# Optimization experiments

Hardware: AMD Instinct MI355X
Metric: run time of the kernel (lower is better)

The kernel has to match this reference:

```python
import jax, jax.numpy as jnp
import numpy as np


def setup_inputs() -> dict:
    key = jax.random.key(0)
    k1, k2 = jax.random.split(key)
    B, C, H, W = 16, 128, 32, 32   # C == embedding_dim
    K = 2048                        # codebook size (num_embeddings)
    x = jax.random.normal(k1, (B, C, H, W), dtype=jnp.float32)
    codebook = jax.random.normal(k2, (K, C), dtype=jnp.float32)
    return {"x": x, "codebook": codebook}


def reference(x, codebook):
    # x: [B, C, H, W] -> NHWC -> flatten to [N, C]
    B, C, H, W = x.shape
    x_nhwc = jnp.transpose(x, (0, 2, 3, 1))
    x_flat = x_nhwc.reshape(-1, C)                      # [N, C]
    # Squared L2 distances via expansion (argmin-equivalent to torch.norm
    # of the broadcast difference, without the [N, K, C] intermediate):
    x_sq = jnp.sum(x_flat * x_flat, axis=1, keepdims=True)   # [N, 1]
    w_sq = jnp.sum(codebook * codebook, axis=1)              # [K]
    d2 = x_sq - 2.0 * (x_flat @ codebook.T) + w_sq           # [N, K]
    encoding_indices = jnp.argmin(d2, axis=1)                # [N]
    encodings = jax.nn.one_hot(encoding_indices, codebook.shape[0],
                               dtype=x_flat.dtype)           # [N, K]
    quantized = encodings @ codebook                         # [N, C]
    quantized = jnp.transpose(quantized.reshape(B, H, W, C), (0, 3, 1, 2))
    return encodings, quantized
```

## Files before the change

### kernel.cpp

```cpp
#include <hip/hip_runtime.h>
#include <hip/hip_bf16.h>

#define N_TOK  16384
#define KCODES 2048
#define CDIM   128
#define BM     64
#define TPB    512
#define NCW    4
#define CPW    (KCODES / NCW)
#define TPW    (CPW / 16)
#define CAP    40
#define DELTA  5.0f
#define ASTR   68

typedef __attribute__((ext_vector_type(8))) short bhalf8;
typedef __attribute__((ext_vector_type(4))) float facc4;

__global__ __launch_bounds__(256) void prep_kernel(const float* __restrict__ cb,
                                                   bhalf8* __restrict__ cbt,
                                                   float* __restrict__ wsq) {
    const int T   = blockIdx.x;
    const int tid = threadIdx.x;
    const int r   = tid >> 4;
    const int g   = tid & 15;
    const float4* src = (const float4*)(cb + ((size_t)(T * 16 + r)) * CDIM + g * 8);
    float4 a0 = src[0], a1 = src[1];

    float s = a0.x*a0.x + a0.y*a0.y + a0.z*a0.z + a0.w*a0.w
            + a1.x*a1.x + a1.y*a1.y + a1.z*a1.z + a1.w*a1.w;
    s += __shfl_xor(s, 1, 64);
    s += __shfl_xor(s, 2, 64);
    s += __shfl_xor(s, 4, 64);
    s += __shfl_xor(s, 8, 64);
    if (g == 0) wsq[T * 16 + r] = s;

    union { unsigned u[4]; bhalf8 v; } fu;
    __hip_bfloat162 h0 = __float22bfloat162_rn(make_float2(a0.x, a0.y));
    __hip_bfloat162 h1 = __float22bfloat162_rn(make_float2(a0.z, a0.w));
    __hip_bfloat162 h2 = __float22bfloat162_rn(make_float2(a1.x, a1.y));
    __hip_bfloat162 h3 = __float22bfloat162_rn(make_float2(a1.z, a1.w));
    fu.u[0] = *(unsigned*)&h0; fu.u[1] = *(unsigned*)&h1;
    fu.u[2] = *(unsigned*)&h2; fu.u[3] = *(unsigned*)&h3;
    const int kf = g >> 2, q = g & 3;
    cbt[(size_t)T * 256 + kf * 64 + q * 16 + r] = fu.v;
}

__global__ __launch_bounds__(TPB, 1) void argmin_kernel(const float* __restrict__ x,
                                                        const float* __restrict__ cb,
                                                        const bhalf8* __restrict__ cbt,
                                                        const float* __restrict__ wsqg,
                                                        float* __restrict__ enc,
                                                        float* __restrict__ quant) {
    __shared__ float As[CDIM][ASTR];
    __shared__ float wsqs[KCODES];
    __shared__ float redvw[NCW][BM];
    __shared__ float rowthr[BM];
    __shared__ int   cnt[BM];
    __shared__ int   candk[BM][CAP];
    __shared__ int   rowidx[BM];

    const int tid  = threadIdx.x;
    const int lane = tid & 63;
    const int w    = tid >> 6;
    const int q    = lane >> 4;
    const int r    = lane & 15;
    const int n0   = blockIdx.x * BM;
    const int b    = n0 >> 10;
    const int hw0  = n0 & 1023;
    const float4 z4 = {0.f, 0.f, 0.f, 0.f};

    {
        int m4 = (tid & 15) << 2;
        int c0 = tid >> 4;
        #pragma unroll
        for (int i = 0; i < 4; i++) {
            int c = c0 + 32 * i;
            float4 v = *(const float4*)(x + (((size_t)(b * CDIM + c)) << 10) + hw0 + m4);
            *(float4*)(&As[c][m4]) = v;
        }
    }
    #pragma unroll
    for (int i = 0; i < KCODES / TPB; i++) wsqs[i * TPB + tid] = wsqg[i * TPB + tid];
    if (tid < BM) cnt[tid] = 0;
    __syncthreads();

    bhalf8 af[4][4];
    if (w < NCW) {
        #pragma unroll
        for (int rt = 0; rt < 4; rt++) {
            int m = rt * 16 + r;
            #pragma unroll
            for (int kf = 0; kf < 4; kf++) {
                union { unsigned u[4]; bhalf8 v; } fu;
                #pragma unroll
                for (int p = 0; p < 4; p++) {
                    int k = kf * 32 + q * 8 + 2 * p;
                    __hip_bfloat162 h = __float22bfloat162_rn(make_float2(As[k][m], As[k + 1][m]));
                    fu.u[p] = *(unsigned*)&h;
                }
                af[rt][kf] = fu.v;
            }
        }
    }

    const int    cw  = w * CPW;
    const size_t tb0 = (size_t)(cw >> 4) * 256;

    if (w < NCW) {
        float rmin[16];
        #pragma unroll
        for (int t = 0; t < 16; t++) rmin[t] = 3.0e38f;

        bhalf8 bcur[4], bnxt[4];
        #pragma unroll
        for (int kf = 0; kf < 4; kf++) bcur[kf] = cbt[tb0 + kf * 64 + lane];
        #pragma unroll
        for (int kf = 0; kf < 4; kf++) bnxt[kf] = cbt[tb0 + 256 + kf * 64 + lane];

        for (int t = 0; t < TPW; t++) {
            bhalf8 bn2[4];
            if (t + 2 < TPW) {
                size_t tb = tb0 + (size_t)(t + 2) * 256;
                #pragma unroll
                for (int kf = 0; kf < 4; kf++) bn2[kf] = cbt[tb + kf * 64 + lane];
            }
            facc4 acc[4];
            #pragma unroll
            for (int rt = 0; rt < 4; rt++) acc[rt] = (facc4){0.f, 0.f, 0.f, 0.f};
            #pragma unroll
            for (int kf = 0; kf < 4; kf++)
                #pragma unroll
                for (int rt = 0; rt < 4; rt++)
                    acc[rt] = __builtin_amdgcn_mfma_f32_16x16x32_bf16(af[rt][kf], bcur[kf], acc[rt], 0, 0, 0);
            float wv = wsqs[cw + t * 16 + r];
            #pragma unroll
            for (int rt = 0; rt < 4; rt++)
                #pragma unroll
                for (int i = 0; i < 4; i++)
                    rmin[rt * 4 + i] = fminf(rmin[rt * 4 + i], fmaf(-2.f, acc[rt][i], wv));
            #pragma unroll
            for (int kf = 0; kf < 4; kf++) { bcur[kf] = bnxt[kf]; bnxt[kf] = bn2[kf]; }
        }
        #pragma unroll
        for (int t = 0; t < 16; t++) {
            float v = rmin[t];
            v = fminf(v, __shfl_xor(v, 1, 64));
            v = fminf(v, __shfl_xor(v, 2, 64));
            v = fminf(v, __shfl_xor(v, 4, 64));
            v = fminf(v, __shfl_xor(v, 8, 64));
            if (r == 0) redvw[w][(t >> 2) * 16 + q * 4 + (t & 3)] = v;
        }
    } else {
        const int f = w - NCW;
        float4* dst = (float4*)(enc + (size_t)(n0 + f * 16) * KCODES);
        #pragma unroll 8
        for (int i = 0; i < 64; i++) dst[(size_t)i * 64 + lane] = z4;
    }
    __syncthreads();
    if (tid < BM) {
        float mv = fminf(fminf(redvw[0][tid], redvw[1][tid]),
                         fminf(redvw[2][tid], redvw[3][tid]));
        rowthr[tid] = mv + DELTA;
    }
    __syncthreads();

    if (w < NCW) {
        float thr[16];
        #pragma unroll
        for (int t = 0; t < 16; t++) thr[t] = rowthr[(t >> 2) * 16 + q * 4 + (t & 3)];

        bhalf8 bcur[4], bnxt[4];
        #pragma unroll
        for (int kf = 0; kf < 4; kf++) bcur[kf] = cbt[tb0 + kf * 64 + lane];
        #pragma unroll
        for (int kf = 0; kf < 4; kf++) bnxt[kf] = cbt[tb0 + 256 + kf * 64 + lane];

        for (int t = 0; t < TPW; t++) {
            bhalf8 bn2[4];
            if (t + 2 < TPW) {
                size_t tb = tb0 + (size_t)(t + 2) * 256;
                #pragma unroll
                for (int kf = 0; kf < 4; kf++) bn2[kf] = cbt[tb + kf * 64 + lane];
            }
            facc4 acc[4];
            #pragma unroll
            for (int rt = 0; rt < 4; rt++) acc[rt] = (facc4){0.f, 0.f, 0.f, 0.f};
            #pragma unroll
            for (int kf = 0; kf < 4; kf++)
                #pragma unroll
                for (int rt = 0; rt < 4; rt++)
                    acc[rt] = __builtin_amdgcn_mfma_f32_16x16x32_bf16(af[rt][kf], bcur[kf], acc[rt], 0, 0, 0);
            float wv = wsqs[cw + t * 16 + r];
            #pragma unroll
            for (int rt = 0; rt < 4; rt++)
                #pragma unroll
                for (int i = 0; i < 4; i++) {
                    float d = fmaf(-2.f, acc[rt][i], wv);
                    if (d <= thr[rt * 4 + i]) {
                        int row = rt * 16 + q * 4 + i;
                        int p = atomicAdd(&cnt[row], 1);
                        if (p < CAP) candk[row][p] = cw + t * 16 + r;
                    }
                }
            #pragma unroll
            for (int kf = 0; kf < 4; kf++) { bcur[kf] = bnxt[kf]; bnxt[kf] = bn2[kf]; }
        }
    } else {
        const int f = w - NCW;
        float4* dst = (float4*)(enc + (size_t)(n0 + f * 16) * KCODES);
        #pragma unroll 8
        for (int i = 64; i < 128; i++) dst[(size_t)i * 64 + lane] = z4;
    }
    __syncthreads();

    for (int m = 8 * w; m < 8 * w + 8; m++) {
        int c = min(cnt[m], CAP);
        float bv = 3.0e38f; int bk = 0x7fffffff;
        for (int t = 0; t < c; t++) {
            int k = candk[m][t];
            float x0 = As[lane][m], x1 = As[lane + 64][m];
            float c0 = cb[(size_t)k * CDIM + lane];
            float c1 = cb[(size_t)k * CDIM + 64 + lane];
            float s = x0 * c0 + x1 * c1;
            #pragma unroll
            for (int off = 1; off <= 32; off <<= 1) s += __shfl_xor(s, off, 64);
            float d = fmaf(-2.f, s, wsqs[k]);
            if (d < bv || (d == bv && k < bk)) { bv = d; bk = k; }
        }
        if (lane == 0) rowidx[m] = bk;
    }
    __syncthreads();

    if (tid < BM) enc[(size_t)(n0 + tid) * KCODES + rowidx[tid]] = 1.0f;

    #pragma unroll
    for (int i = tid; i < BM * CDIM / 4; i += TPB) {
        int c  = i >> 4;
        int hq = (i & 15) << 2;
        float4 v;
        v.x = cb[(size_t)rowidx[hq + 0] * CDIM + c];
        v.y = cb[(size_t)rowidx[hq + 1] * CDIM + c];
        v.z = cb[(size_t)rowidx[hq + 2] * CDIM + c];
        v.w = cb[(size_t)rowidx[hq + 3] * CDIM + c];
        *(float4*)(quant + (((size_t)(b * CDIM + c)) << 10) + hw0 + hq) = v;
    }
}

extern "C" void kernel_launch(void* const* d_in, const int* in_sizes, int n_in,
                              void* d_out, int out_size, void* d_ws, size_t ws_size,
                              hipStream_t stream) {
    const float* x  = (const float*)d_in[0];
    const float* cb = (const float*)d_in[1];
    float* out = (float*)d_out;

    bhalf8* cbt  = (bhalf8*)d_ws;
    float*  wsqp = (float*)((char*)d_ws + 512 * 1024);

    prep_kernel<<<KCODES / 16, 256, 0, stream>>>(cb, cbt, wsqp);
    argmin_kernel<<<N_TOK / BM, TPB, 0, stream>>>(x, cb, cbt, wsqp,
                                                  out, out + (size_t)N_TOK * KCODES);
}
```

Baseline: 191.3 us.

## Decouple zero-fill waves from compute waves with shared-memory flags instead of block barriers

The four zero-fill waves now write the whole one-hot matrix with nontemporal stores, then spin on a shared flag and write the ones themselves. The compute waves sync only among themselves through atomic counters, so the fill no longer stalls them at block barriers. The change also deepens codebook prefetch to four tiles with a fully unrolled loop and computes fp32 refinement distances one candidate per lane rather than with shuffle reductions. In exchange it relies on spin-waits in shared memory, raises register pressure, and lifts the candidate cap with more shared memory.

```diff
diff --git a/kernel.cpp b/kernel.cpp
--- a/kernel.cpp
+++ b/kernel.cpp
@@ -9,12 +9,13 @@
 #define NCW    4
 #define CPW    (KCODES / NCW)
 #define TPW    (CPW / 16)
-#define CAP    40
+#define CAP    48
 #define DELTA  5.0f
 #define ASTR   68
 
 typedef __attribute__((ext_vector_type(8))) short bhalf8;
 typedef __attribute__((ext_vector_type(4))) float facc4;
+typedef __attribute__((ext_vector_type(4))) float nf4;
 
 __global__ __launch_bounds__(256) void prep_kernel(const float* __restrict__ cb,
                                                    bhalf8* __restrict__ cbt,
@@ -54,10 +55,11 @@
     __shared__ float As[CDIM][ASTR];
     __shared__ float wsqs[KCODES];
     __shared__ float redvw[NCW][BM];
-    __shared__ float rowthr[BM];
     __shared__ int   cnt[BM];
     __shared__ int   candk[BM][CAP];
+    __shared__ float candd[BM][CAP];
     __shared__ int   rowidx[BM];
+    __shared__ int   cflag0, cflag1, cflag2, rflag;
 
     const int tid  = threadIdx.x;
     const int lane = tid & 63;
@@ -67,63 +69,77 @@
     const int n0   = blockIdx.x * BM;
     const int b    = n0 >> 10;
     const int hw0  = n0 & 1023;
-    const float4 z4 = {0.f, 0.f, 0.f, 0.f};
+
+    if (tid < BM) cnt[tid] = 0;
+    if (tid == 0) { cflag0 = 0; cflag1 = 0; cflag2 = 0; rflag = 0; }
+    __syncthreads();
+
+    if (w >= NCW) {
+        const int f = w - NCW;
+        nf4* dst = (nf4*)(enc + (size_t)(n0 + f * 16) * KCODES);
+        const nf4 z4 = {0.f, 0.f, 0.f, 0.f};
+        #pragma unroll 8
+        for (int i = 0; i < 128; i++)
+            __builtin_nontemporal_store(z4, dst + (size_t)i * 64 + lane);
+        __threadfence();
+        while (*(volatile int*)&rflag < NCW) __builtin_amdgcn_s_sleep(2);
+        __threadfence_block();
+        if (lane < 16) {
+            int m = f * 16 + lane;
+            enc[(size_t)(n0 + m) * KCODES + rowidx[m]] = 1.0f;
+        }
+        return;
+    }
 
     {
         int m4 = (tid & 15) << 2;
         int c0 = tid >> 4;
         #pragma unroll
-        for (int i = 0; i < 4; i++) {
-            int c = c0 + 32 * i;
+        for (int i = 0; i < 8; i++) {
+            int c = c0 + 16 * i;
             float4 v = *(const float4*)(x + (((size_t)(b * CDIM + c)) << 10) + hw0 + m4);
             *(float4*)(&As[c][m4]) = v;
         }
-    }
-    #pragma unroll
-    for (int i = 0; i < KCODES / TPB; i++) wsqs[i * TPB + tid] = wsqg[i * TPB + tid];
-    if (tid < BM) cnt[tid] = 0;
-    __syncthreads();
+        #pragma unroll
+        for (int i = 0; i < 8; i++) wsqs[i * 256 + tid] = wsqg[i * 256 + tid];
+    }
+    __threadfence_block();
+    if (lane == 0) atomicAdd(&cflag0, 1);
+    while (*(volatile int*)&cflag0 < NCW) __builtin_amdgcn_s_sleep(1);
+    __threadfence_block();
 
     bhalf8 af[4][4];
-    if (w < NCW) {
-        #pragma unroll
-        for (int rt = 0; rt < 4; rt++) {
-            int m = rt * 16 + r;
-            #pragma unroll
-            for (int kf = 0; kf < 4; kf++) {
-                union { unsigned u[4]; bhalf8 v; } fu;
-                #pragma unroll
-                for (int p = 0; p < 4; p++) {
-                    int k = kf * 32 + q * 8 + 2 * p;
-                    __hip_bfloat162 h = __float22bfloat162_rn(make_float2(As[k][m], As[k + 1][m]));
-                    fu.u[p] = *(unsigned*)&h;
-                }
-                af[rt][kf] = fu.v;
-            }
+    #pragma unroll
+    for (int rt = 0; rt < 4; rt++) {
+        int m = rt * 16 + r;
+        #pragma unroll
+        for (int kf = 0; kf < 4; kf++) {
+            union { unsigned u[4]; bhalf8 v; } fu;
+            #pragma unroll
+            for (int p = 0; p < 4; p++) {
+                int k = kf * 32 + q * 8 + 2 * p;
+                __hip_bfloat162 h = __float22bfloat162_rn(make_float2(As[k][m], As[k + 1][m]));
+                fu.u[p] = *(unsigned*)&h;
+            }
+            af[rt][kf] = fu.v;
         }
     }
 
     const int    cw  = w * CPW;
     const size_t tb0 = (size_t)(cw >> 4) * 256;
 
-    if (w < NCW) {
-        float rmin[16];
-        #pragma unroll
-        for (int t = 0; t < 16; t++) rmin[t] = 3.0e38f;
-
-        bhalf8 bcur[4], bnxt[4];
-        #pragma unroll
-        for (int kf = 0; kf < 4; kf++) bcur[kf] = cbt[tb0 + kf * 64 + lane];
-        #pragma unroll
-        for (int kf = 0; kf < 4; kf++) bnxt[kf] = cbt[tb0 + 256 + kf * 64 + lane];
-
+    float rmin[16];
+    #pragma unroll
+    for (int t = 0; t < 16; t++) rmin[t] = 3.0e38f;
+    {
+        bhalf8 bb[4][4];
+        #pragma unroll
+        for (int d = 0; d < 4; d++)
+            #pragma unroll
+            for (int kf = 0; kf < 4; kf++)
+                bb[d][kf] = cbt[tb0 + (size_t)d * 256 + kf * 64 + lane];
+        #pragma unroll
         for (int t = 0; t < TPW; t++) {
-            bhalf8 bn2[4];
-            if (t + 2 < TPW) {
-                size_t tb = tb0 + (size_t)(t + 2) * 256;
-                #pragma unroll
-                for (int kf = 0; kf < 4; kf++) bn2[kf] = cbt[tb + kf * 64 + lane];
-            }
             facc4 acc[4];
             #pragma unroll
             for (int rt = 0; rt < 4; rt++) acc[rt] = (facc4){0.f, 0.f, 0.f, 0.f};
@@ -131,57 +147,51 @@
             for (int kf = 0; kf < 4; kf++)
                 #pragma unroll
                 for (int rt = 0; rt < 4; rt++)
-                    acc[rt] = __builtin_amdgcn_mfma_f32_16x16x32_bf16(af[rt][kf], bcur[kf], acc[rt], 0, 0, 0);
+                    acc[rt] = __builtin_amdgcn_mfma_f32_16x16x32_bf16(af[rt][kf], bb[t & 3][kf], acc[rt], 0, 0, 0);
             float wv = wsqs[cw + t * 16 + r];
             #pragma unroll
             for (int rt = 0; rt < 4; rt++)
                 #pragma unroll
                 for (int i = 0; i < 4; i++)
                     rmin[rt * 4 + i] = fminf(rmin[rt * 4 + i], fmaf(-2.f, acc[rt][i], wv));
-            #pragma unroll
-            for (int kf = 0; kf < 4; kf++) { bcur[kf] = bnxt[kf]; bnxt[kf] = bn2[kf]; }
-        }
-        #pragma unroll
-        for (int t = 0; t < 16; t++) {
-            float v = rmin[t];
-            v = fminf(v, __shfl_xor(v, 1, 64));
-            v = fminf(v, __shfl_xor(v, 2, 64));
-            v = fminf(v, __shfl_xor(v, 4, 64));
-            v = fminf(v, __shfl_xor(v, 8, 64));
-            if (r == 0) redvw[w][(t >> 2) * 16 + q * 4 + (t & 3)] = v;
-        }
-    } else {
-        const int f = w - NCW;
-        float4* dst = (float4*)(enc + (size_t)(n0 + f * 16) * KCODES);
-        #pragma unroll 8
-        for (int i = 0; i < 64; i++) dst[(size_t)i * 64 + lane] = z4;
-    }
-    __syncthreads();
-    if (tid < BM) {
-        float mv = fminf(fminf(redvw[0][tid], redvw[1][tid]),
-                         fminf(redvw[2][tid], redvw[3][tid]));
-        rowthr[tid] = mv + DELTA;
-    }
-    __syncthreads();
-
-    if (w < NCW) {
-        float thr[16];
-        #pragma unroll
-        for (int t = 0; t < 16; t++) thr[t] = rowthr[(t >> 2) * 16 + q * 4 + (t & 3)];
-
-        bhalf8 bcur[4], bnxt[4];
-        #pragma unroll
-        for (int kf = 0; kf < 4; kf++) bcur[kf] = cbt[tb0 + kf * 64 + lane];
-        #pragma unroll
-        for (int kf = 0; kf < 4; kf++) bnxt[kf] = cbt[tb0 + 256 + kf * 64 + lane];
-
+            if (t + 4 < TPW) {
+                #pragma unroll
+                for (int kf = 0; kf < 4; kf++)
+                    bb[t & 3][kf] = cbt[tb0 + (size_t)(t + 4) * 256 + kf * 64 + lane];
+            }
+        }
+    }
+    #pragma unroll
+    for (int t = 0; t < 16; t++) {
+        float v = rmin[t];
+        v = fminf(v, __shfl_xor(v, 1, 64));
+        v = fminf(v, __shfl_xor(v, 2, 64));
+        v = fminf(v, __shfl_xor(v, 4, 64));
+        v = fminf(v, __shfl_xor(v, 8, 64));
+        if (r == 0) redvw[w][(t >> 2) * 16 + q * 4 + (t & 3)] = v;
+    }
+    __threadfence_block();
+    if (lane == 0) atomicAdd(&cflag1, 1);
+    while (*(volatile int*)&cflag1 < NCW) __builtin_amdgcn_s_sleep(1);
+    __threadfence_block();
+
+    float thr[16];
+    #pragma unroll
+    for (int t = 0; t < 16; t++) {
+        int rm = (t >> 2) * 16 + q * 4 + (t & 3);
+        thr[t] = fminf(fminf(redvw[0][rm], redvw[1][rm]),
+                       fminf(redvw[2][rm], redvw[3][rm])) + DELTA;
+    }
+
+    {
+        bhalf8 bb[4][4];
+        #pragma unroll
+        for (int d = 0; d < 4; d++)
+            #pragma unroll
+            for (int kf = 0; kf < 4; kf++)
+                bb[d][kf] = cbt[tb0 + (size_t)d * 256 + kf * 64 + lane];
+        #pragma unroll
         for (int t = 0; t < TPW; t++) {
-            bhalf8 bn2[4];
-            if (t + 2 < TPW) {
-                size_t tb = tb0 + (size_t)(t + 2) * 256;
-                #pragma unroll
-                for (int kf = 0; kf < 4; kf++) bn2[kf] = cbt[tb + kf * 64 + lane];
-            }
             facc4 acc[4];
             #pragma unroll
             for (int rt = 0; rt < 4; rt++) acc[rt] = (facc4){0.f, 0.f, 0.f, 0.f};
@@ -189,7 +199,7 @@
             for (int kf = 0; kf < 4; kf++)
                 #pragma unroll
                 for (int rt = 0; rt < 4; rt++)
-                    acc[rt] = __builtin_amdgcn_mfma_f32_16x16x32_bf16(af[rt][kf], bcur[kf], acc[rt], 0, 0, 0);
+                    acc[rt] = __builtin_amdgcn_mfma_f32_16x16x32_bf16(af[rt][kf], bb[t & 3][kf], acc[rt], 0, 0, 0);
             float wv = wsqs[cw + t * 16 + r];
             #pragma unroll
             for (int rt = 0; rt < 4; rt++)
@@ -202,47 +212,72 @@
                         if (p < CAP) candk[row][p] = cw + t * 16 + r;
                     }
                 }
-            #pragma unroll
-            for (int kf = 0; kf < 4; kf++) { bcur[kf] = bnxt[kf]; bnxt[kf] = bn2[kf]; }
-        }
-    } else {
-        const int f = w - NCW;
-        float4* dst = (float4*)(enc + (size_t)(n0 + f * 16) * KCODES);
-        #pragma unroll 8
-        for (int i = 64; i < 128; i++) dst[(size_t)i * 64 + lane] = z4;
-    }
-    __syncthreads();
-
-    for (int m = 8 * w; m < 8 * w + 8; m++) {
-        int c = min(cnt[m], CAP);
+            if (t + 4 < TPW) {
+                #pragma unroll
+                for (int kf = 0; kf < 4; kf++)
+                    bb[t & 3][kf] = cbt[tb0 + (size_t)(t + 4) * 256 + kf * 64 + lane];
+            }
+        }
+    }
+    __threadfence_block();
+    if (lane == 0) atomicAdd(&cflag2, 1);
+    while (*(volatile int*)&cflag2 < NCW) __builtin_amdgcn_s_sleep(1);
+    __threadfence_block();
+
+    const int m0 = 16 * w;
+    int cnts[16], offs[16], tot = 0;
+    #pragma unroll
+    for (int j = 0; j < 16; j++) {
+        int c = min(cnt[m0 + j], CAP);
+        offs[j] = tot; tot += c; cnts[j] = c;
+    }
+    for (int base = 0; base < tot; base += 64) {
+        int ci = base + lane;
+        if (ci < tot) {
+            int j = 0;
+            #pragma unroll
+            for (int jj = 1; jj < 16; jj++) if (ci >= offs[jj]) j = jj;
+            int row  = m0 + j;
+            int slot = ci - offs[j];
+            int k    = candk[row][slot];
+            const float4* cr = (const float4*)(cb + (size_t)k * CDIM);
+            float s = 0.f;
+            #pragma unroll
+            for (int c4 = 0; c4 < 32; c4++) {
+                float4 v = cr[c4];
+                s = fmaf(As[4 * c4 + 0][row], v.x, s);
+                s = fmaf(As[4 * c4 + 1][row], v.y, s);
+                s = fmaf(As[4 * c4 + 2][row], v.z, s);
+                s = fmaf(As[4 * c4 + 3][row], v.w, s);
+            }
+            candd[row][slot] = fmaf(-2.f, s, wsqs[k]);
+        }
+    }
+    __threadfence_block();
+    if (lane < 16) {
+        int row = m0 + lane;
         float bv = 3.0e38f; int bk = 0x7fffffff;
-        for (int t = 0; t < c; t++) {
-            int k = candk[m][t];
-            float x0 = As[lane][m], x1 = As[lane + 64][m];
-            float c0 = cb[(size_t)k * CDIM + lane];
-            float c1 = cb[(size_t)k * CDIM + 64 + lane];
-            float s = x0 * c0 + x1 * c1;
-            #pragma unroll
-            for (int off = 1; off <= 32; off <<= 1) s += __shfl_xor(s, off, 64);
-            float d = fmaf(-2.f, s, wsqs[k]);
+        for (int t = 0; t < cnts[lane]; t++) {
+            float d = candd[row][t];
+            int   k = candk[row][t];
             if (d < bv || (d == bv && k < bk)) { bv = d; bk = k; }
         }
-        if (lane == 0) rowidx[m] = bk;
-    }
-    __syncthreads();
-
-    if (tid < BM) enc[(size_t)(n0 + tid) * KCODES + rowidx[tid]] = 1.0f;
-
-    #pragma unroll
-    for (int i = tid; i < BM * CDIM / 4; i += TPB) {
-        int c  = i >> 4;
-        int hq = (i & 15) << 2;
+        rowidx[row] = bk;
+    }
+    __threadfence_block();
+    if (lane == 0) atomicAdd(&rflag, 1);
+
+    #pragma unroll
+    for (int i = 0; i < 8; i++) {
+        int c  = i * 16 + (lane >> 2);
+        int f4 = lane & 3;
+        int mb = m0 + 4 * f4;
         float4 v;
-        v.x = cb[(size_t)rowidx[hq + 0] * CDIM + c];
-        v.y = cb[(size_t)rowidx[hq + 1] * CDIM + c];
-        v.z = cb[(size_t)rowidx[hq + 2] * CDIM + c];
-        v.w = cb[(size_t)rowidx[hq + 3] * CDIM + c];
-        *(float4*)(quant + (((size_t)(b * CDIM + c)) << 10) + hw0 + hq) = v;
+        v.x = cb[(size_t)rowidx[mb + 0] * CDIM + c];
+        v.y = cb[(size_t)rowidx[mb + 1] * CDIM + c];
+        v.z = cb[(size_t)rowidx[mb + 2] * CDIM + c];
+        v.w = cb[(size_t)rowidx[mb + 3] * CDIM + c];
+        *(float4*)(quant + (((size_t)(b * CDIM + c)) << 10) + hw0 + mb) = v;
     }
 }
 
```

Measured after the change: 360.2 us. +88.2%, slower.
